# Kernel optimization log

Measured on AMD Instinct MI355X. Metric: run time of the kernel, lower is better.

Reference implementation:

```python
import jax, jax.numpy as jnp
import numpy as np

D_MODEL = 256
NUM_HEADS = 4
EPS = 1e-6


def setup_inputs() -> dict:
    key = jax.random.key(0)
    ks = jax.random.split(key, 9)
    B, T, D = 4, 2048, D_MODEL
    scale = 1.0 / np.sqrt(D)
    inp = {
        "x": jax.random.normal(ks[0], (B, T, D), dtype=jnp.float32),
        "Wq": jax.random.normal(ks[1], (D, D), dtype=jnp.float32) * scale,
        "bq": jnp.zeros((D,), dtype=jnp.float32),
        "Wk": jax.random.normal(ks[2], (D, D), dtype=jnp.float32) * scale,
        "bk": jnp.zeros((D,), dtype=jnp.float32),
        "Wv": jax.random.normal(ks[3], (D, D), dtype=jnp.float32) * scale,
        "bv": jnp.zeros((D,), dtype=jnp.float32),
        "Wo": jax.random.normal(ks[4], (D, D), dtype=jnp.float32) * scale,
        "bo": jnp.zeros((D,), dtype=jnp.float32),
    }
    return inp


def _feature_map(a):
    # F.elu(x) + 1.0
    return jax.nn.elu(a) + 1.0


def reference(x, Wq, bq, Wk, bk, Wv, bv, Wo, bo):
    B, T, D = x.shape
    H = NUM_HEADS
    dh = D // H
    Q = _feature_map((x @ Wq + bq).reshape(B, T, H, dh))
    K = _feature_map((x @ Wk + bk).reshape(B, T, H, dh))
    V = (x @ Wv + bv).reshape(B, T, H, dh)
    # outer-product state: (B,T,H,dh,dh), cumulative over time
    KV = jnp.einsum('bthd,bthm->bthdm', K, V)
    S = jnp.cumsum(KV, axis=1)
    Z = jnp.cumsum(K, axis=1)
    out = jnp.einsum('bthd,bthdm->bthm', Q, S)
    denom = jnp.einsum('bthd,bthd->bth', Q, Z)[..., None] + EPS
    out = (out / denom).reshape(B, T, D)
    return out @ Wo + bo
```

## Files before the change

### kernel.cpp

```cpp
#include <hip/hip_runtime.h>
#include <hip/hip_bf16.h>

#define D_MODEL 256
#define NHEADS 4
#define DHEAD 64
#define BATCH 4
#define TSEQ 2048
#define CHUNK 64
#define NCHUNK (TSEQ / CHUNK)
#define NTOK (BATCH * TSEQ)
#define NBH (BATCH * NHEADS)
#define EPSV 1e-6f

typedef __bf16 bf16x8 __attribute__((ext_vector_type(8)));
typedef float f32x4 __attribute__((ext_vector_type(4)));

__device__ __forceinline__ float elu1(float a) {
    return a > 0.0f ? a + 1.0f : __expf(a);
}

__device__ __forceinline__ unsigned short f2bf(float f) {
    __hip_bfloat16 h = __float2bfloat16(f);
    return __builtin_bit_cast(unsigned short, h);
}

__device__ __forceinline__ float bf2f(unsigned short u) {
    return __bfloat162float(__builtin_bit_cast(__hip_bfloat16, u));
}

__device__ __forceinline__ void fma4(float4& o, float a, const float4& v) {
    o.x = fmaf(a, v.x, o.x);
    o.y = fmaf(a, v.y, o.y);
    o.z = fmaf(a, v.z, o.z);
    o.w = fmaf(a, v.w, o.w);
}

__device__ __forceinline__ void mask4(float4& a, int s, int t0) {
    if (s > t0 + 0) a.x = 0.f;
    if (s > t0 + 1) a.y = 0.f;
    if (s > t0 + 2) a.z = 0.f;
    if (s > t0 + 3) a.w = 0.f;
}

__device__ __forceinline__ void gld_lds16(const void* g, void* l) {
    __builtin_amdgcn_global_load_lds(
        (const __attribute__((address_space(1))) void*)g,
        (__attribute__((address_space(3))) void*)l, 16, 0, 0);
}

__global__ __launch_bounds__(256) void convert_x_kernel(
    const float* __restrict__ x, unsigned short* __restrict__ xb)
{
    const int i = (blockIdx.x * 256 + threadIdx.x) * 8;
    const float4 a = *reinterpret_cast<const float4*>(&x[i]);
    const float4 b = *reinterpret_cast<const float4*>(&x[i + 4]);
    ushort4 u0 = { f2bf(a.x), f2bf(a.y), f2bf(a.z), f2bf(a.w) };
    ushort4 u1 = { f2bf(b.x), f2bf(b.y), f2bf(b.z), f2bf(b.w) };
    *reinterpret_cast<ushort4*>(&xb[i]) = u0;
    *reinterpret_cast<ushort4*>(&xb[i + 4]) = u1;
}

__global__ __launch_bounds__(256) void convert_w_kernel(
    const float* __restrict__ Wq, const float* __restrict__ Wk,
    const float* __restrict__ Wv, const float* __restrict__ Wo,
    unsigned short* __restrict__ Wt, unsigned short* __restrict__ Wot)
{
    __shared__ float Ls[64][65];
    const int tid = threadIdx.x;
    const int wi = blockIdx.x >> 4;
    const int ti = blockIdx.x & 15;
    const int k0 = (ti >> 2) * 64, n0 = (ti & 3) * 64;
    const float* W = wi == 0 ? Wq : wi == 1 ? Wk : wi == 2 ? Wv : Wo;
#pragma unroll
    for (int i = 0; i < 16; ++i) {
        const int idx = i * 256 + tid;
        const int r = idx >> 6, c = idx & 63;
        Ls[r][c] = W[(size_t)(k0 + r) * D_MODEL + n0 + c];
    }
    __syncthreads();
    unsigned short* outp = (wi < 3) ? (Wt + (size_t)(wi * 256 + n0) * D_MODEL + k0)
                                    : (Wot + (size_t)n0 * D_MODEL + k0);
#pragma unroll
    for (int i = 0; i < 16; ++i) {
        const int idx = i * 256 + tid;
        const int rn = idx >> 6, ck = idx & 63;
        outp[(size_t)rn * D_MODEL + ck] = f2bf(Ls[ck][rn]);
    }
}

template<int MODE>
__global__ __launch_bounds__(256) void mfma_gemm_kernel(
    const unsigned short* __restrict__ A,
    const unsigned short* __restrict__ Bt,
    const float* __restrict__ b0, const float* __restrict__ b1,
    const float* __restrict__ b2,
    void* __restrict__ O0, void* __restrict__ O1, void* __restrict__ O2)
{
    __shared__ __align__(16) unsigned short As[128 * 64];
    __shared__ __align__(16) unsigned short Bs[128 * 64];
    const int tid = threadIdx.x;
    const int wave = tid >> 6, lane = tid & 63;
    const int la = lane & 15, q = lane >> 4;
    const int wm = (wave >> 1) * 64, wn = (wave & 1) * 64;

    int mtile, ntile;
    if (MODE == 0) { ntile = blockIdx.x % 6; mtile = blockIdx.x / 6; }
    else           { ntile = blockIdx.x & 1; mtile = blockIdx.x >> 1; }
    const int m0 = mtile * 128, n0 = ntile * 128;

    const unsigned short* Ab = A  + (size_t)m0 * D_MODEL;
    const unsigned short* Bb = Bt + (size_t)n0 * D_MODEL;

    f32x4 acc[4][4];
#pragma unroll
    for (int i = 0; i < 4; ++i)
#pragma unroll
        for (int j = 0; j < 4; ++j) acc[i][j] = (f32x4){0.f, 0.f, 0.f, 0.f};

    for (int k0 = 0; k0 < D_MODEL; k0 += 64) {
#pragma unroll
        for (int i = 0; i < 4; ++i) {
            const int bslot = i * 256 + wave * 64;
            const int slot = bslot + lane;
            const int m = slot >> 3, s = slot & 7;
            const int g = s ^ (m & 7);
            gld_lds16(Ab + (size_t)m * D_MODEL + k0 + g * 8, &As[bslot * 8]);
            gld_lds16(Bb + (size_t)m * D_MODEL + k0 + g * 8, &Bs[bslot * 8]);
        }
        __syncthreads();

        bf16x8 af[4][2], bfr[4][2];
#pragma unroll
        for (int i = 0; i < 4; ++i) {
#pragma unroll
            for (int kh = 0; kh < 2; ++kh) {
                const int g = kh * 4 + q;
                const int m = wm + i * 16 + la;
                af[i][kh] = *reinterpret_cast<const bf16x8*>(
                    &As[m * 64 + ((g ^ (m & 7)) << 3)]);
                const int n = wn + i * 16 + la;
                bfr[i][kh] = *reinterpret_cast<const bf16x8*>(
                    &Bs[n * 64 + ((g ^ (n & 7)) << 3)]);
            }
        }
#pragma unroll
        for (int mi = 0; mi < 4; ++mi)
#pragma unroll
            for (int ni = 0; ni < 4; ++ni) {
                acc[mi][ni] = __builtin_amdgcn_mfma_f32_16x16x32_bf16(
                    af[mi][0], bfr[ni][0], acc[mi][ni], 0, 0, 0);
                acc[mi][ni] = __builtin_amdgcn_mfma_f32_16x16x32_bf16(
                    af[mi][1], bfr[ni][1], acc[mi][ni], 0, 0, 0);
            }
        __syncthreads();
    }

#pragma unroll
    for (int mi = 0; mi < 4; ++mi) {
#pragma unroll
        for (int ni = 0; ni < 4; ++ni) {
            const int row = m0 + wm + mi * 16 + q * 4;
            const int col = n0 + wn + ni * 16 + la;
            if (MODE == 0) {
                const int which = col >> 8;
                const int cl = col & 255;
                unsigned short* Out = (unsigned short*)
                    (which == 0 ? O0 : which == 1 ? O1 : O2);
                const float* bias = which == 0 ? b0 : which == 1 ? b1 : b2;
                const int act = (which < 2);
                const float bv = bias[cl];
#pragma unroll
                for (int r = 0; r < 4; ++r) {
                    float v = acc[mi][ni][r] + bv;
                    if (act) v = elu1(v);
                    Out[(size_t)(row + r) * D_MODEL + cl] = f2bf(v);
                }
            } else {
                float* Out = (float*)O0;
                const float bv = b0[col];
#pragma unroll
                for (int r = 0; r < 4; ++r)
                    Out[(size_t)(row + r) * D_MODEL + col] = acc[mi][ni][r] + bv;
            }
        }
    }
}

__global__ __launch_bounds__(256) void chunksum_kernel(
    const unsigned short* __restrict__ Kb, const unsigned short* __restrict__ Vb,
    float* __restrict__ P, float* __restrict__ Zc)
{
    const int tid = threadIdx.x;
    const int c  = blockIdx.x % NCHUNK;
    const int bh = blockIdx.x / NCHUNK;
    const int b = bh / NHEADS, h = bh % NHEADS;

    __shared__ float Ks[CHUNK][DHEAD + 4];
    __shared__ float Vs[CHUNK][DHEAD];

    const size_t gbase = ((size_t)(b * TSEQ + c * CHUNK)) * D_MODEL + h * DHEAD;
#pragma unroll
    for (int i = 0; i < 16; ++i) {
        const int idx = i * 256 + tid;
        const int t = idx >> 6, d = idx & 63;
        Ks[t][d] = bf2f(Kb[gbase + (size_t)t * D_MODEL + d]);
        Vs[t][d] = bf2f(Vb[gbase + (size_t)t * D_MODEL + d]);
    }
    __syncthreads();

    const int ty = tid >> 4, tx = tid & 15;
    const int d0 = ty * 4, m0 = tx * 4;
    float4 o0 = {0,0,0,0}, o1 = o0, o2 = o0, o3 = o0;
    for (int t = 0; t < CHUNK; ++t) {
        const float4 k4 = *reinterpret_cast<const float4*>(&Ks[t][d0]);
        const float4 v4 = *reinterpret_cast<const float4*>(&Vs[t][m0]);
        fma4(o0, k4.x, v4);
        fma4(o1, k4.y, v4);
        fma4(o2, k4.z, v4);
        fma4(o3, k4.w, v4);
    }
    float* kvb = P + (size_t)blockIdx.x * (DHEAD * DHEAD);
    *reinterpret_cast<float4*>(&kvb[(d0 + 0) * DHEAD + m0]) = o0;
    *reinterpret_cast<float4*>(&kvb[(d0 + 1) * DHEAD + m0]) = o1;
    *reinterpret_cast<float4*>(&kvb[(d0 + 2) * DHEAD + m0]) = o2;
    *reinterpret_cast<float4*>(&kvb[(d0 + 3) * DHEAD + m0]) = o3;

    if (tid < DHEAD) {
        float z = 0.f;
        for (int t = 0; t < CHUNK; ++t) z += Ks[t][tid];
        Zc[(size_t)blockIdx.x * DHEAD + tid] = z;
    }
}

__global__ __launch_bounds__(256) void prefix_kernel(
    float* __restrict__ P, float* __restrict__ Zc)
{
    const int tid = threadIdx.x;
    if (blockIdx.x < NBH * 16) {
        const int bh = blockIdx.x >> 4;
        const int e = ((blockIdx.x & 15) << 8) + tid;
        const size_t base = (size_t)bh * NCHUNK * (DHEAD * DHEAD) + e;
        float v[NCHUNK];
#pragma unroll
        for (int c = 0; c < NCHUNK; ++c) v[c] = P[base + (size_t)c * (DHEAD * DHEAD)];
        float s = 0.f;
#pragma unroll
        for (int c = 0; c < NCHUNK; ++c) {
            const float t = v[c];
            P[base + (size_t)c * (DHEAD * DHEAD)] = s;
            s += t;
        }
    } else {
        const int j = ((int)(blockIdx.x - NBH * 16) << 8) + tid;
        if (j < NBH * DHEAD) {
            const int bh = j >> 6, d = j & 63;
            float v[NCHUNK];
#pragma unroll
            for (int c = 0; c < NCHUNK; ++c) v[c] = Zc[(bh * NCHUNK + c) * DHEAD + d];
            float s = 0.f;
#pragma unroll
            for (int c = 0; c < NCHUNK; ++c) {
                const float t = v[c];
                Zc[(bh * NCHUNK + c) * DHEAD + d] = s;
                s += t;
            }
        }
    }
}

__global__ __launch_bounds__(256) void chunkout_kernel(
    const unsigned short* __restrict__ Qb, const unsigned short* __restrict__ Kb,
    const unsigned short* __restrict__ Vb,
    const float* __restrict__ Sx, const float* __restrict__ Zx,
    unsigned short* __restrict__ Ob)
{
    const int tid = threadIdx.x;
    const int c  = blockIdx.x % NCHUNK;
    const int bh = blockIdx.x / NCHUNK;
    const int b = bh / NHEADS, h = bh % NHEADS;

    __shared__ float Qt[DHEAD][CHUNK + 4];
    __shared__ float KtAt[DHEAD][CHUNK + 4];
    __shared__ float Vs[CHUNK][DHEAD];
    __shared__ float Ss[DHEAD][DHEAD];
    __shared__ float zsh[DHEAD];
    __shared__ float dnm[CHUNK];

    const size_t gbase = ((size_t)(b * TSEQ + c * CHUNK)) * D_MODEL + h * DHEAD;
    const size_t sbase = (size_t)blockIdx.x * (DHEAD * DHEAD);
#pragma unroll
    for (int i = 0; i < 16; ++i) {
        const int idx = i * 256 + tid;
        const int t = idx >> 6, d = idx & 63;
        Qt[d][t]   = bf2f(Qb[gbase + (size_t)t * D_MODEL + d]);
        KtAt[d][t] = bf2f(Kb[gbase + (size_t)t * D_MODEL + d]);
        Vs[t][d]   = bf2f(Vb[gbase + (size_t)t * D_MODEL + d]);
        Ss[t][d]   = Sx[sbase + idx];
    }
    if (tid < DHEAD) zsh[tid] = Zx[((size_t)bh * NCHUNK + c) * DHEAD + tid];
    __syncthreads();

    const int ty = tid >> 4, tx = tid & 15;
    const int t0 = ty * 4, s0 = tx * 4;

    float4 a0 = {0,0,0,0}, a1 = a0, a2 = a0, a3 = a0;
    for (int d = 0; d < DHEAD; ++d) {
        const float4 q4 = *reinterpret_cast<const float4*>(&Qt[d][t0]);
        const float4 k4 = *reinterpret_cast<const float4*>(&KtAt[d][s0]);
        fma4(a0, k4.x, q4);
        fma4(a1, k4.y, q4);
        fma4(a2, k4.z, q4);
        fma4(a3, k4.w, q4);
    }
    mask4(a0, s0 + 0, t0);
    mask4(a1, s0 + 1, t0);
    mask4(a2, s0 + 2, t0);
    mask4(a3, s0 + 3, t0);
    __syncthreads();
    *reinterpret_cast<float4*>(&KtAt[s0 + 0][t0]) = a0;
    *reinterpret_cast<float4*>(&KtAt[s0 + 1][t0]) = a1;
    *reinterpret_cast<float4*>(&KtAt[s0 + 2][t0]) = a2;
    *reinterpret_cast<float4*>(&KtAt[s0 + 3][t0]) = a3;
    __syncthreads();

    if (tid < CHUNK) {
        float dv = 0.f;
        for (int s = 0; s < CHUNK; ++s) dv += KtAt[s][tid];
        for (int d = 0; d < DHEAD; ++d) dv = fmaf(Qt[d][tid], zsh[d], dv);
        dnm[tid] = dv + EPSV;
    }
    __syncthreads();

    const int m0 = tx * 4;
    float4 o0 = {0,0,0,0}, o1 = o0, o2 = o0, o3 = o0;
    for (int d = 0; d < DHEAD; ++d) {
        const float4 q4 = *reinterpret_cast<const float4*>(&Qt[d][t0]);
        const float4 s4 = *reinterpret_cast<const float4*>(&Ss[d][m0]);
        fma4(o0, q4.x, s4);
        fma4(o1, q4.y, s4);
        fma4(o2, q4.z, s4);
        fma4(o3, q4.w, s4);
    }
    for (int s = 0; s < CHUNK; ++s) {
        const float4 a4 = *reinterpret_cast<const float4*>(&KtAt[s][t0]);
        const float4 v4 = *reinterpret_cast<const float4*>(&Vs[s][m0]);
        fma4(o0, a4.x, v4);
        fma4(o1, a4.y, v4);
        fma4(o2, a4.z, v4);
        fma4(o3, a4.w, v4);
    }
    const float r0 = 1.f / dnm[t0 + 0];
    const float r1 = 1.f / dnm[t0 + 1];
    const float r2 = 1.f / dnm[t0 + 2];
    const float r3 = 1.f / dnm[t0 + 3];
    ushort4 p0 = { f2bf(o0.x * r0), f2bf(o0.y * r0), f2bf(o0.z * r0), f2bf(o0.w * r0) };
    ushort4 p1 = { f2bf(o1.x * r1), f2bf(o1.y * r1), f2bf(o1.z * r1), f2bf(o1.w * r1) };
    ushort4 p2 = { f2bf(o2.x * r2), f2bf(o2.y * r2), f2bf(o2.z * r2), f2bf(o2.w * r2) };
    ushort4 p3 = { f2bf(o3.x * r3), f2bf(o3.y * r3), f2bf(o3.z * r3), f2bf(o3.w * r3) };
    *reinterpret_cast<ushort4*>(&Ob[gbase + (size_t)(t0 + 0) * D_MODEL + m0]) = p0;
    *reinterpret_cast<ushort4*>(&Ob[gbase + (size_t)(t0 + 1) * D_MODEL + m0]) = p1;
    *reinterpret_cast<ushort4*>(&Ob[gbase + (size_t)(t0 + 2) * D_MODEL + m0]) = p2;
    *reinterpret_cast<ushort4*>(&Ob[gbase + (size_t)(t0 + 3) * D_MODEL + m0]) = p3;
}

extern "C" void kernel_launch(void* const* d_in, const int* in_sizes, int n_in,
                              void* d_out, int out_size, void* d_ws, size_t ws_size,
                              hipStream_t stream)
{
    const float* x  = (const float*)d_in[0];
    const float* Wq = (const float*)d_in[1];
    const float* bq = (const float*)d_in[2];
    const float* Wk = (const float*)d_in[3];
    const float* bk = (const float*)d_in[4];
    const float* Wv = (const float*)d_in[5];
    const float* bv = (const float*)d_in[6];
    const float* Wo = (const float*)d_in[7];
    const float* bo = (const float*)d_in[8];
    float* out = (float*)d_out;

    const size_t NE = (size_t)NTOK * D_MODEL;
    unsigned short* xb  = (unsigned short*)d_ws;
    unsigned short* Wt  = xb + NE;
    unsigned short* Wot = Wt + 768 * 256;
    unsigned short* Qb  = Wot + 256 * 256;
    unsigned short* Kb  = Qb + NE;
    unsigned short* Vb  = Kb + NE;
    unsigned short* Ob  = Vb + NE;
    float* P = (float*)(Ob + NE);
    float* Z = P + (size_t)NBH * NCHUNK * DHEAD * DHEAD;

    convert_x_kernel<<<NTOK * D_MODEL / 8 / 256, 256, 0, stream>>>(x, xb);
    convert_w_kernel<<<64, 256, 0, stream>>>(Wq, Wk, Wv, Wo, Wt, Wot);
    mfma_gemm_kernel<0><<<(NTOK / 128) * 6, 256, 0, stream>>>(
        xb, Wt, bq, bk, bv, Qb, Kb, Vb);
    chunksum_kernel<<<NBH * NCHUNK, 256, 0, stream>>>(Kb, Vb, P, Z);
    prefix_kernel<<<NBH * 16 + 4, 256, 0, stream>>>(P, Z);
    chunkout_kernel<<<NBH * NCHUNK, 256, 0, stream>>>(Qb, Kb, Vb, P, Z, Ob);
    mfma_gemm_kernel<1><<<(NTOK / 128) * 2, 256, 0, stream>>>(
        Ob, Wot, bo, nullptr, nullptr, out, nullptr, nullptr);
}
```

Measured before the change: 122.9 us.

## Use bf16 MFMA for chunk state sums and intra-chunk attention outputs

Replaces the scalar FP32 FMA loops in chunksum_kernel and chunkout_kernel with bf16 16x16x32 MFMA instructions, converting LDS fp32 tiles to bf16 fragments on the fly. The KV chunk state is now stored transposed (V-major), so chunkout reads it directly from global memory as the B operand instead of staging it in LDS. LDS layouts change to padded row-major/transposed tiles to fit the MFMA fragment loads. This adds bf16 rounding of the intermediate state and attention scores, which reduces accuracy, and the per-lane global reads of the state may be less coalesced.

After: 117.0 us. -4.9%, faster.

```diff
diff --git a/kernel.cpp b/kernel.cpp
--- a/kernel.cpp
+++ b/kernel.cpp
@@ -11,9 +11,11 @@
 #define NTOK (BATCH * TSEQ)
 #define NBH (BATCH * NHEADS)
 #define EPSV 1e-6f
+#define LSTRF 68
 
 typedef __bf16 bf16x8 __attribute__((ext_vector_type(8)));
 typedef float f32x4 __attribute__((ext_vector_type(4)));
+typedef unsigned short us8 __attribute__((ext_vector_type(8)));
 
 __device__ __forceinline__ float elu1(float a) {
     return a > 0.0f ? a + 1.0f : __expf(a);
@@ -28,18 +30,13 @@
     return __bfloat162float(__builtin_bit_cast(__hip_bfloat16, u));
 }
 
-__device__ __forceinline__ void fma4(float4& o, float a, const float4& v) {
-    o.x = fmaf(a, v.x, o.x);
-    o.y = fmaf(a, v.y, o.y);
-    o.z = fmaf(a, v.z, o.z);
-    o.w = fmaf(a, v.w, o.w);
-}
-
-__device__ __forceinline__ void mask4(float4& a, int s, int t0) {
-    if (s > t0 + 0) a.x = 0.f;
-    if (s > t0 + 1) a.y = 0.f;
-    if (s > t0 + 2) a.z = 0.f;
-    if (s > t0 + 3) a.w = 0.f;
+__device__ __forceinline__ bf16x8 frag8(const float* p) {
+    const float4 x = *reinterpret_cast<const float4*>(p);
+    const float4 y = *reinterpret_cast<const float4*>(p + 4);
+    us8 u;
+    u[0] = f2bf(x.x); u[1] = f2bf(x.y); u[2] = f2bf(x.z); u[3] = f2bf(x.w);
+    u[4] = f2bf(y.x); u[5] = f2bf(y.y); u[6] = f2bf(y.z); u[7] = f2bf(y.w);
+    return __builtin_bit_cast(bf16x8, u);
 }
 
 __device__ __forceinline__ void gld_lds16(const void* g, void* l) {
@@ -188,46 +185,63 @@
 
 __global__ __launch_bounds__(256) void chunksum_kernel(
     const unsigned short* __restrict__ Kb, const unsigned short* __restrict__ Vb,
-    float* __restrict__ P, float* __restrict__ Zc)
-{
+    float* __restrict__ Pt, float* __restrict__ Zc)
+{
+    __shared__ float Ktf[DHEAD * LSTRF];
+    __shared__ float Vtf[DHEAD * LSTRF];
     const int tid = threadIdx.x;
     const int c  = blockIdx.x % NCHUNK;
     const int bh = blockIdx.x / NCHUNK;
     const int b = bh / NHEADS, h = bh % NHEADS;
-
-    __shared__ float Ks[CHUNK][DHEAD + 4];
-    __shared__ float Vs[CHUNK][DHEAD];
-
     const size_t gbase = ((size_t)(b * TSEQ + c * CHUNK)) * D_MODEL + h * DHEAD;
+
 #pragma unroll
     for (int i = 0; i < 16; ++i) {
         const int idx = i * 256 + tid;
         const int t = idx >> 6, d = idx & 63;
-        Ks[t][d] = bf2f(Kb[gbase + (size_t)t * D_MODEL + d]);
-        Vs[t][d] = bf2f(Vb[gbase + (size_t)t * D_MODEL + d]);
+        Ktf[d * LSTRF + t] = bf2f(Kb[gbase + (size_t)t * D_MODEL + d]);
+        Vtf[d * LSTRF + t] = bf2f(Vb[gbase + (size_t)t * D_MODEL + d]);
     }
     __syncthreads();
 
-    const int ty = tid >> 4, tx = tid & 15;
-    const int d0 = ty * 4, m0 = tx * 4;
-    float4 o0 = {0,0,0,0}, o1 = o0, o2 = o0, o3 = o0;
-    for (int t = 0; t < CHUNK; ++t) {
-        const float4 k4 = *reinterpret_cast<const float4*>(&Ks[t][d0]);
-        const float4 v4 = *reinterpret_cast<const float4*>(&Vs[t][m0]);
-        fma4(o0, k4.x, v4);
-        fma4(o1, k4.y, v4);
-        fma4(o2, k4.z, v4);
-        fma4(o3, k4.w, v4);
-    }
-    float* kvb = P + (size_t)blockIdx.x * (DHEAD * DHEAD);
-    *reinterpret_cast<float4*>(&kvb[(d0 + 0) * DHEAD + m0]) = o0;
-    *reinterpret_cast<float4*>(&kvb[(d0 + 1) * DHEAD + m0]) = o1;
-    *reinterpret_cast<float4*>(&kvb[(d0 + 2) * DHEAD + m0]) = o2;
-    *reinterpret_cast<float4*>(&kvb[(d0 + 3) * DHEAD + m0]) = o3;
+    const int wave = tid >> 6, lane = tid & 63;
+    const int la = lane & 15, q = lane >> 4;
+    const int wm = (wave >> 1) * 32, wn = (wave & 1) * 32;
+
+    f32x4 acc[2][2];
+#pragma unroll
+    for (int i = 0; i < 2; ++i)
+#pragma unroll
+        for (int j = 0; j < 2; ++j) acc[i][j] = (f32x4){0.f, 0.f, 0.f, 0.f};
+
+#pragma unroll
+    for (int ks = 0; ks < 2; ++ks) {
+        const int ko = ks * 32 + q * 8;
+        const bf16x8 a0  = frag8(&Vtf[(wm + la) * LSTRF + ko]);
+        const bf16x8 a1  = frag8(&Vtf[(wm + 16 + la) * LSTRF + ko]);
+        const bf16x8 bb0 = frag8(&Ktf[(wn + la) * LSTRF + ko]);
+        const bf16x8 bb1 = frag8(&Ktf[(wn + 16 + la) * LSTRF + ko]);
+        acc[0][0] = __builtin_amdgcn_mfma_f32_16x16x32_bf16(a0, bb0, acc[0][0], 0, 0, 0);
+        acc[0][1] = __builtin_amdgcn_mfma_f32_16x16x32_bf16(a0, bb1, acc[0][1], 0, 0, 0);
+        acc[1][0] = __builtin_amdgcn_mfma_f32_16x16x32_bf16(a1, bb0, acc[1][0], 0, 0, 0);
+        acc[1][1] = __builtin_amdgcn_mfma_f32_16x16x32_bf16(a1, bb1, acc[1][1], 0, 0, 0);
+    }
+
+    float* Pb = Pt + (size_t)blockIdx.x * (DHEAD * DHEAD);
+#pragma unroll
+    for (int mi = 0; mi < 2; ++mi)
+#pragma unroll
+        for (int ni = 0; ni < 2; ++ni) {
+            const int row = wm + mi * 16 + q * 4;
+            const int col = wn + ni * 16 + la;
+#pragma unroll
+            for (int r = 0; r < 4; ++r)
+                Pb[(row + r) * DHEAD + col] = acc[mi][ni][r];
+        }
 
     if (tid < DHEAD) {
         float z = 0.f;
-        for (int t = 0; t < CHUNK; ++t) z += Ks[t][tid];
+        for (int t = 0; t < CHUNK; ++t) z += Ktf[tid * LSTRF + t];
         Zc[(size_t)blockIdx.x * DHEAD + tid] = z;
     }
 }
@@ -271,96 +285,120 @@
 __global__ __launch_bounds__(256) void chunkout_kernel(
     const unsigned short* __restrict__ Qb, const unsigned short* __restrict__ Kb,
     const unsigned short* __restrict__ Vb,
-    const float* __restrict__ Sx, const float* __restrict__ Zx,
+    const float* __restrict__ Pt, const float* __restrict__ Zx,
     unsigned short* __restrict__ Ob)
 {
+    __shared__ float Qs[CHUNK * LSTRF];
+    __shared__ float Ks[CHUNK * LSTRF];
+    __shared__ float Vtf[DHEAD * LSTRF];
+    __shared__ float At[CHUNK * LSTRF];
+    __shared__ float zsh[DHEAD];
+    __shared__ float dnm[CHUNK];
+
     const int tid = threadIdx.x;
     const int c  = blockIdx.x % NCHUNK;
     const int bh = blockIdx.x / NCHUNK;
     const int b = bh / NHEADS, h = bh % NHEADS;
-
-    __shared__ float Qt[DHEAD][CHUNK + 4];
-    __shared__ float KtAt[DHEAD][CHUNK + 4];
-    __shared__ float Vs[CHUNK][DHEAD];
-    __shared__ float Ss[DHEAD][DHEAD];
-    __shared__ float zsh[DHEAD];
-    __shared__ float dnm[CHUNK];
-
     const size_t gbase = ((size_t)(b * TSEQ + c * CHUNK)) * D_MODEL + h * DHEAD;
-    const size_t sbase = (size_t)blockIdx.x * (DHEAD * DHEAD);
+    const float* Pp = Pt + (size_t)blockIdx.x * (DHEAD * DHEAD);
+
 #pragma unroll
     for (int i = 0; i < 16; ++i) {
         const int idx = i * 256 + tid;
         const int t = idx >> 6, d = idx & 63;
-        Qt[d][t]   = bf2f(Qb[gbase + (size_t)t * D_MODEL + d]);
-        KtAt[d][t] = bf2f(Kb[gbase + (size_t)t * D_MODEL + d]);
-        Vs[t][d]   = bf2f(Vb[gbase + (size_t)t * D_MODEL + d]);
-        Ss[t][d]   = Sx[sbase + idx];
+        const float qv = bf2f(Qb[gbase + (size_t)t * D_MODEL + d]);
+        const float kv = bf2f(Kb[gbase + (size_t)t * D_MODEL + d]);
+        const float vv = bf2f(Vb[gbase + (size_t)t * D_MODEL + d]);
+        Qs[t * LSTRF + d]  = qv;
+        Ks[t * LSTRF + d]  = kv;
+        Vtf[d * LSTRF + t] = vv;
     }
     if (tid < DHEAD) zsh[tid] = Zx[((size_t)bh * NCHUNK + c) * DHEAD + tid];
     __syncthreads();
 
-    const int ty = tid >> 4, tx = tid & 15;
-    const int t0 = ty * 4, s0 = tx * 4;
-
-    float4 a0 = {0,0,0,0}, a1 = a0, a2 = a0, a3 = a0;
-    for (int d = 0; d < DHEAD; ++d) {
-        const float4 q4 = *reinterpret_cast<const float4*>(&Qt[d][t0]);
-        const float4 k4 = *reinterpret_cast<const float4*>(&KtAt[d][s0]);
-        fma4(a0, k4.x, q4);
-        fma4(a1, k4.y, q4);
-        fma4(a2, k4.z, q4);
-        fma4(a3, k4.w, q4);
-    }
-    mask4(a0, s0 + 0, t0);
-    mask4(a1, s0 + 1, t0);
-    mask4(a2, s0 + 2, t0);
-    mask4(a3, s0 + 3, t0);
-    __syncthreads();
-    *reinterpret_cast<float4*>(&KtAt[s0 + 0][t0]) = a0;
-    *reinterpret_cast<float4*>(&KtAt[s0 + 1][t0]) = a1;
-    *reinterpret_cast<float4*>(&KtAt[s0 + 2][t0]) = a2;
-    *reinterpret_cast<float4*>(&KtAt[s0 + 3][t0]) = a3;
+    const int wave = tid >> 6, lane = tid & 63;
+    const int la = lane & 15, q = lane >> 4;
+    const int wt = (wave >> 1) * 32, wn = (wave & 1) * 32;
+
+    f32x4 acc[2][2];
+#pragma unroll
+    for (int i = 0; i < 2; ++i)
+#pragma unroll
+        for (int j = 0; j < 2; ++j) acc[i][j] = (f32x4){0.f, 0.f, 0.f, 0.f};
+#pragma unroll
+    for (int ks = 0; ks < 2; ++ks) {
+        const int ko = ks * 32 + q * 8;
+        const bf16x8 a0  = frag8(&Qs[(wt + la) * LSTRF + ko]);
+        const bf16x8 a1  = frag8(&Qs[(wt + 16 + la) * LSTRF + ko]);
+        const bf16x8 bb0 = frag8(&Ks[(wn + la) * LSTRF + ko]);
+        const bf16x8 bb1 = frag8(&Ks[(wn + 16 + la) * LSTRF + ko]);
+        acc[0][0] = __builtin_amdgcn_mfma_f32_16x16x32_bf16(a0, bb0, acc[0][0], 0, 0, 0);
+        acc[0][1] = __builtin_amdgcn_mfma_f32_16x16x32_bf16(a0, bb1, acc[0][1], 0, 0, 0);
+        acc[1][0] = __builtin_amdgcn_mfma_f32_16x16x32_bf16(a1, bb0, acc[1][0], 0, 0, 0);
+        acc[1][1] = __builtin_amdgcn_mfma_f32_16x16x32_bf16(a1, bb1, acc[1][1], 0, 0, 0);
+    }
+#pragma unroll
+    for (int mi = 0; mi < 2; ++mi)
+#pragma unroll
+        for (int ni = 0; ni < 2; ++ni) {
+            const int t0 = wt + mi * 16 + q * 4;
+            const int s  = wn + ni * 16 + la;
+#pragma unroll
+            for (int r = 0; r < 4; ++r)
+                At[(t0 + r) * LSTRF + s] = (s <= t0 + r) ? acc[mi][ni][r] : 0.f;
+        }
     __syncthreads();
 
     if (tid < CHUNK) {
         float dv = 0.f;
-        for (int s = 0; s < CHUNK; ++s) dv += KtAt[s][tid];
-        for (int d = 0; d < DHEAD; ++d) dv = fmaf(Qt[d][tid], zsh[d], dv);
+        for (int s = 0; s < CHUNK; ++s) dv += At[tid * LSTRF + s];
+        for (int d = 0; d < DHEAD; ++d) dv = fmaf(Qs[tid * LSTRF + d], zsh[d], dv);
         dnm[tid] = dv + EPSV;
     }
     __syncthreads();
 
-    const int m0 = tx * 4;
-    float4 o0 = {0,0,0,0}, o1 = o0, o2 = o0, o3 = o0;
-    for (int d = 0; d < DHEAD; ++d) {
-        const float4 q4 = *reinterpret_cast<const float4*>(&Qt[d][t0]);
-        const float4 s4 = *reinterpret_cast<const float4*>(&Ss[d][m0]);
-        fma4(o0, q4.x, s4);
-        fma4(o1, q4.y, s4);
-        fma4(o2, q4.z, s4);
-        fma4(o3, q4.w, s4);
-    }
-    for (int s = 0; s < CHUNK; ++s) {
-        const float4 a4 = *reinterpret_cast<const float4*>(&KtAt[s][t0]);
-        const float4 v4 = *reinterpret_cast<const float4*>(&Vs[s][m0]);
-        fma4(o0, a4.x, v4);
-        fma4(o1, a4.y, v4);
-        fma4(o2, a4.z, v4);
-        fma4(o3, a4.w, v4);
-    }
-    const float r0 = 1.f / dnm[t0 + 0];
-    const float r1 = 1.f / dnm[t0 + 1];
-    const float r2 = 1.f / dnm[t0 + 2];
-    const float r3 = 1.f / dnm[t0 + 3];
-    ushort4 p0 = { f2bf(o0.x * r0), f2bf(o0.y * r0), f2bf(o0.z * r0), f2bf(o0.w * r0) };
-    ushort4 p1 = { f2bf(o1.x * r1), f2bf(o1.y * r1), f2bf(o1.z * r1), f2bf(o1.w * r1) };
-    ushort4 p2 = { f2bf(o2.x * r2), f2bf(o2.y * r2), f2bf(o2.z * r2), f2bf(o2.w * r2) };
-    ushort4 p3 = { f2bf(o3.x * r3), f2bf(o3.y * r3), f2bf(o3.z * r3), f2bf(o3.w * r3) };
-    *reinterpret_cast<ushort4*>(&Ob[gbase + (size_t)(t0 + 0) * D_MODEL + m0]) = p0;
-    *reinterpret_cast<ushort4*>(&Ob[gbase + (size_t)(t0 + 1) * D_MODEL + m0]) = p1;
-    *reinterpret_cast<ushort4*>(&Ob[gbase + (size_t)(t0 + 2) * D_MODEL + m0]) = p2;
-    *reinterpret_cast<ushort4*>(&Ob[gbase + (size_t)(t0 + 3) * D_MODEL + m0]) = p3;
+    f32x4 o[2][2];
+#pragma unroll
+    for (int i = 0; i < 2; ++i)
+#pragma unroll
+        for (int j = 0; j < 2; ++j) o[i][j] = (f32x4){0.f, 0.f, 0.f, 0.f};
+#pragma unroll
+    for (int ks = 0; ks < 2; ++ks) {
+        const int ko = ks * 32 + q * 8;
+        const bf16x8 a0  = frag8(&Qs[(wt + la) * LSTRF + ko]);
+        const bf16x8 a1  = frag8(&Qs[(wt + 16 + la) * LSTRF + ko]);
+        const bf16x8 bb0 = frag8(&Pp[(wn + la) * DHEAD + ko]);
+        const bf16x8 bb1 = frag8(&Pp[(wn + 16 + la) * DHEAD + ko]);
+        o[0][0] = __builtin_amdgcn_mfma_f32_16x16x32_bf16(a0, bb0, o[0][0], 0, 0, 0);
+        o[0][1] = __builtin_amdgcn_mfma_f32_16x16x32_bf16(a0, bb1, o[0][1], 0, 0, 0);
+        o[1][0] = __builtin_amdgcn_mfma_f32_16x16x32_bf16(a1, bb0, o[1][0], 0, 0, 0);
+        o[1][1] = __builtin_amdgcn_mfma_f32_16x16x32_bf16(a1, bb1, o[1][1], 0, 0, 0);
+    }
+#pragma unroll
+    for (int ks = 0; ks < 2; ++ks) {
+        const int ko = ks * 32 + q * 8;
+        const bf16x8 a0  = frag8(&At[(wt + la) * LSTRF + ko]);
+        const bf16x8 a1  = frag8(&At[(wt + 16 + la) * LSTRF + ko]);
+        const bf16x8 bb0 = frag8(&Vtf[(wn + la) * LSTRF + ko]);
+        const bf16x8 bb1 = frag8(&Vtf[(wn + 16 + la) * LSTRF + ko]);
+        o[0][0] = __builtin_amdgcn_mfma_f32_16x16x32_bf16(a0, bb0, o[0][0], 0, 0, 0);
+        o[0][1] = __builtin_amdgcn_mfma_f32_16x16x32_bf16(a0, bb1, o[0][1], 0, 0, 0);
+        o[1][0] = __builtin_amdgcn_mfma_f32_16x16x32_bf16(a1, bb0, o[1][0], 0, 0, 0);
+        o[1][1] = __builtin_amdgcn_mfma_f32_16x16x32_bf16(a1, bb1, o[1][1], 0, 0, 0);
+    }
+
+#pragma unroll
+    for (int mi = 0; mi < 2; ++mi)
+#pragma unroll
+        for (int ni = 0; ni < 2; ++ni) {
+            const int t0 = wt + mi * 16 + q * 4;
+            const int m  = wn + ni * 16 + la;
+#pragma unroll
+            for (int r = 0; r < 4; ++r) {
+                const float v = o[mi][ni][r] / dnm[t0 + r];
+                Ob[gbase + (size_t)(t0 + r) * D_MODEL + m] = f2bf(v);
+            }
+        }
 }
 
 extern "C" void kernel_launch(void* const* d_in, const int* in_sizes, int n_in,
```
